# Kernel tuning notes

Hardware: AMD Instinct MI355X
Metric: run time of the kernel (lower is better)

The kernel has to match this reference:

```python
import jax, jax.numpy as jnp
import numpy as np

B, Q, K, H = 4, 256, 256, 512
NEG = -1e9


def setup_inputs() -> dict:
    key = jax.random.key(0)
    ks = jax.random.split(key, 7)
    scale = 1.0 / np.sqrt(H)
    return {
        "query": jax.random.normal(ks[0], (B, Q, H), jnp.float32),
        "key": jax.random.normal(ks[1], (B, K, H), jnp.float32),
        "value": jax.random.normal(ks[2], (B, K, H), jnp.float32),
        "valid_lens": jax.random.randint(ks[3], (B,), 0, K, jnp.int32),
        "Wq": jax.random.normal(ks[4], (H, H), jnp.float32) * scale,
        "Wk": jax.random.normal(ks[5], (H, H), jnp.float32) * scale,
        "wv": jax.random.normal(ks[6], (H,), jnp.float32) * scale,
    }


def reference(query, key, value, valid_lens, Wq, Wk, wv):
    # projections (nn.Linear without bias)
    q = query @ Wq              # [B,Q,H]
    k = key @ Wk                # [B,K,H]
    # broadcast add + tanh: [B,Q,K,H]
    features = jnp.tanh(q[:, :, None, :] + k[:, None, :, :])
    # score projection w_v: [B,Q,K]
    scores = jnp.einsum("bqkh,h->bqk", features, wv)
    # sequence mask: positions >= valid_len masked out
    mask = jnp.arange(K)[None, :] >= valid_lens[:, None]   # [B,K]
    scores = jnp.where(mask[:, None, :], NEG, scores)
    attn = jax.nn.softmax(scores, axis=-1)                 # [B,Q,K]
    context = jnp.einsum("bqk,bkh->bqh", attn, value)      # [B,Q,H]
    return context
```

## Files before the change

kernel.cpp:

```cpp
#include <hip/hip_runtime.h>
#include <hip/hip_bf16.h>

#define B_ 4
#define Q_ 256
#define K_ 256
#define H_ 512
#define NEG (-1e9f)
#define PRESCALE 2.885390081777927f

typedef _Float16 half8 __attribute__((ext_vector_type(8)));
typedef float    f32x4 __attribute__((ext_vector_type(4)));

__global__ __launch_bounds__(512) void proj_kernel(
    const float* __restrict__ Xq, const float* __restrict__ Xk,
    const float* __restrict__ Wq, const float* __restrict__ Wk,
    float* __restrict__ Eq, float* __restrict__ EkT,
    const int* __restrict__ vlen)
{
    const int bx   = blockIdx.x;
    const int z    = bx >> 4;
    const int row0 = (bx & 15) * 64;
    const int bb   = row0 >> 8;
    const int k0   = row0 & 255;
    if (z && k0 >= vlen[bb]) return;

    const float* X = z ? Xk : Xq;
    const float* W = z ? Wk : Wq;

    __shared__ _Float16 Xl[2][8 * 520];
    __shared__ _Float16 Wl[2][8 * 520];

    const int col0 = blockIdx.y * 64;
    const int t    = threadIdx.x;
    const int lane = t & 63;
    const int wave = t >> 6;
    const int mw   = wave >> 1;
    const int nw   = wave & 1;
    const int m    = lane & 15;
    const int kgl  = lane >> 4;

    const int xr = t >> 3;
    const int xg = t & 7;
    const int wc = t & 63;
    const int wg = t >> 6;

    f32x4 acc[2] = {};

    float4 xv0 = *(const float4*)&X[(size_t)(row0 + xr) * H_ + xg * 8];
    float4 xv1 = *(const float4*)&X[(size_t)(row0 + xr) * H_ + xg * 8 + 4];
    float wv8[8];
    #pragma unroll
    for (int i = 0; i < 8; ++i)
        wv8[i] = W[(size_t)(wg * 8 + i) * H_ + col0 + wc];

    for (int it = 0; it < 8; ++it) {
        const int buf = it & 1;
        {
            half8 hx;
            hx[0] = (_Float16)xv0.x; hx[1] = (_Float16)xv0.y;
            hx[2] = (_Float16)xv0.z; hx[3] = (_Float16)xv0.w;
            hx[4] = (_Float16)xv1.x; hx[5] = (_Float16)xv1.y;
            hx[6] = (_Float16)xv1.z; hx[7] = (_Float16)xv1.w;
            *(half8*)&Xl[buf][xg * 520 + xr * 8] = hx;
            half8 hw;
            #pragma unroll
            for (int i = 0; i < 8; ++i) hw[i] = (_Float16)wv8[i];
            *(half8*)&Wl[buf][wg * 520 + wc * 8] = hw;
        }
        __syncthreads();
        if (it < 7) {
            const int kk = (it + 1) * 64;
            xv0 = *(const float4*)&X[(size_t)(row0 + xr) * H_ + kk + xg * 8];
            xv1 = *(const float4*)&X[(size_t)(row0 + xr) * H_ + kk + xg * 8 + 4];
            #pragma unroll
            for (int i = 0; i < 8; ++i)
                wv8[i] = W[(size_t)(kk + wg * 8 + i) * H_ + col0 + wc];
        }
        const _Float16* Asrc = z ? &Wl[buf][0] : &Xl[buf][0];
        const _Float16* Bsrc = z ? &Xl[buf][0] : &Wl[buf][0];
        #pragma unroll
        for (int ks = 0; ks < 2; ++ks) {
            const int slab = (ks * 4 + kgl) * 520;
            const half8 af = *(const half8*)&Asrc[slab + (16 * mw + m) * 8];
            #pragma unroll
            for (int nt = 0; nt < 2; ++nt) {
                const half8 bf =
                    *(const half8*)&Bsrc[slab + (nw * 32 + nt * 16 + m) * 8];
                acc[nt] = __builtin_amdgcn_mfma_f32_16x16x32_f16(af, bf, acc[nt], 0, 0, 0);
            }
        }
    }

    const int rloc = 16 * mw + kgl * 4;
    if (!z) {
        #pragma unroll
        for (int nt = 0; nt < 2; ++nt) {
            const int gcol = col0 + nw * 32 + nt * 16 + m;
            #pragma unroll
            for (int r = 0; r < 4; ++r)
                Eq[(size_t)(row0 + rloc + r) * H_ + gcol] =
                    __builtin_amdgcn_exp2f(acc[nt][r] * PRESCALE);
        }
    } else {
        #pragma unroll
        for (int nt = 0; nt < 2; ++nt) {
            const int gk = k0 + nw * 32 + nt * 16 + m;
            #pragma unroll
            for (int r = 0; r < 4; ++r)
                EkT[((size_t)bb * H_ + col0 + rloc + r) * K_ + gk] =
                    __builtin_amdgcn_exp2f(acc[nt][r] * PRESCALE);
        }
    }
}

__global__ __launch_bounds__(512) void fused_attn(
    const float* __restrict__ Eq, const float* __restrict__ EkT,
    const float* __restrict__ value, const int* __restrict__ vlen,
    const float* __restrict__ wv, float* __restrict__ out)
{
    const int qt = blockIdx.x;
    const int b  = blockIdx.y;
    const int q0 = qt * 2;
    const int t    = threadIdx.x;
    const int wave = t >> 6;
    const int lane = t & 63;

    __shared__ float eqh2[8 * 132];
    __shared__ float wm2[8 * 68];
    __shared__ float sc[2][K_];
    __shared__ float ctxp[4][2][H_];

    const int valid = vlen[b];

    if (t < 256) {
        const int qi = t >> 7, p4 = (t & 127) * 4;
        const float4 v = *(const float4*)&Eq[((size_t)b * Q_ + q0 + qi) * H_ + p4];
        const float vv[4] = {v.x, v.y, v.z, v.w};
        #pragma unroll
        for (int j = 0; j < 4; ++j) {
            const int h = p4 + j;
            eqh2[(h & 7) * 132 + (h >> 3) * 2 + qi] = vv[j];
        }
    } else if (t < 384) {
        const int i = (t - 256) * 4;
        const float4 w = *(const float4*)&wv[i];
        const float ww[4] = {w.x, w.y, w.z, w.w};
        #pragma unroll
        for (int j = 0; j < 4; ++j) {
            const int h = i + j;
            wm2[(h & 7) * 68 + (h >> 3)] = -2.f * ww[j];
        }
    }
    __syncthreads();

    const int band = wave * 32;
    const int ho   = lane >> 3;
    const int kg   = lane & 7;
    const int kq   = band + kg * 4;

    if (band < valid) {
        const float* ekp = EkT + ((size_t)b * H_ + ho) * K_ + kq;
        float a0[4] = {}, a1[4] = {};
        float4 pe[4], n1[4], n2[4];
        #pragma unroll
        for (int p = 0; p < 4; ++p)
            pe[p] = *(const float4*)(ekp + (size_t)p * 8 * K_);
        #pragma unroll
        for (int p = 0; p < 4; ++p)
            n1[p] = *(const float4*)(ekp + (size_t)(4 + p) * 8 * K_);

        for (int g = 0; g < 16; ++g) {
            if (g < 14) {
                #pragma unroll
                for (int p = 0; p < 4; ++p)
                    n2[p] = *(const float4*)(ekp + (size_t)((g + 2) * 4 + p) * 8 * K_);
            }
            const float4 eqA = *(const float4*)&eqh2[ho * 132 + g * 8];
            const float4 eqB = *(const float4*)&eqh2[ho * 132 + g * 8 + 4];
            const float4 wv4 = *(const float4*)&wm2[ho * 68 + g * 4];
            const float eq0[4] = {eqA.x, eqA.z, eqB.x, eqB.z};
            const float eq1[4] = {eqA.y, eqA.w, eqB.y, eqB.w};
            const float wmp[4] = {wv4.x, wv4.y, wv4.z, wv4.w};
            #pragma unroll
            for (int p = 0; p < 4; ++p) {
                const float ek4[4] = {pe[p].x, pe[p].y, pe[p].z, pe[p].w};
                #pragma unroll
                for (int j = 0; j < 4; ++j) {
                    const float g0 = __builtin_fmaf(eq0[p], ek4[j], 1.0f);
                    a0[j] = __builtin_fmaf(wmp[p], __builtin_amdgcn_rcpf(g0), a0[j]);
                    const float g1 = __builtin_fmaf(eq1[p], ek4[j], 1.0f);
                    a1[j] = __builtin_fmaf(wmp[p], __builtin_amdgcn_rcpf(g1), a1[j]);
                }
            }
            #pragma unroll
            for (int p = 0; p < 4; ++p) { pe[p] = n1[p]; n1[p] = n2[p]; }
        }
        #pragma unroll
        for (int d = 8; d < 64; d <<= 1) {
            #pragma unroll
            for (int j = 0; j < 4; ++j) {
                a0[j] += __shfl_xor(a0[j], d);
                a1[j] += __shfl_xor(a1[j], d);
            }
        }
        if (ho == 0) {
            *(float4*)&sc[0][kq] = make_float4(a0[0], a0[1], a0[2], a0[3]);
            *(float4*)&sc[1][kq] = make_float4(a1[0], a1[1], a1[2], a1[3]);
        }
    }
    __syncthreads();

    if (wave < 2) {
        const int q = wave;
        if (valid == 0) {
            #pragma unroll
            for (int j = 0; j < 4; ++j) sc[q][lane + 64 * j] = 1.0f / K_;
        } else {
            float sv[4], mx = -3e38f;
            #pragma unroll
            for (int j = 0; j < 4; ++j) {
                const int kk = lane + 64 * j;
                const float s = (kk < valid) ? sc[q][kk] : NEG;
                sv[j] = s;
                mx = fmaxf(mx, s);
            }
            #pragma unroll
            for (int d = 32; d; d >>= 1) mx = fmaxf(mx, __shfl_xor(mx, d));
            float ev[4], sum = 0.f;
            #pragma unroll
            for (int j = 0; j < 4; ++j) { ev[j] = __expf(sv[j] - mx); sum += ev[j]; }
            #pragma unroll
            for (int d = 32; d; d >>= 1) sum += __shfl_xor(sum, d);
            const float inv = 1.0f / sum;
            #pragma unroll
            for (int j = 0; j < 4; ++j) sc[q][lane + 64 * j] = ev[j] * inv;
        }
    }
    __syncthreads();

    const int klim = (valid == 0) ? K_ : valid;
    const int kb   = wave * 32;
    const int kend = min(32, klim - kb);
    const int h0   = lane * 8;

    float c0[8] = {}, c1[8] = {};
    for (int kc = 0; kc < kend; ++kc) {
        const int kk = kb + kc;
        const float4* vp = (const float4*)&value[((size_t)b * K_ + kk) * H_ + h0];
        const float4 v0 = vp[0], v1 = vp[1];
        const float vr[8] = {v0.x, v0.y, v0.z, v0.w, v1.x, v1.y, v1.z, v1.w};
        const float a0 = sc[0][kk], a1 = sc[1][kk];
        #pragma unroll
        for (int j = 0; j < 8; ++j) {
            c0[j] = __builtin_fmaf(a0, vr[j], c0[j]);
            c1[j] = __builtin_fmaf(a1, vr[j], c1[j]);
        }
    }

    #define PARK(s)                                                         \
        do {                                                                \
            float* d0 = &ctxp[s][0][h0];                                    \
            float* d1 = &ctxp[s][1][h0];                                    \
            ((float4*)d0)[0] = make_float4(c0[0], c0[1], c0[2], c0[3]);     \
            ((float4*)d0)[1] = make_float4(c0[4], c0[5], c0[6], c0[7]);     \
            ((float4*)d1)[0] = make_float4(c1[0], c1[1], c1[2], c1[3]);     \
            ((float4*)d1)[1] = make_float4(c1[4], c1[5], c1[6], c1[7]);     \
        } while (0)
    #define FOLD(s)                                                         \
        do {                                                                \
            const float* d0 = &ctxp[s][0][h0];                              \
            const float* d1 = &ctxp[s][1][h0];                              \
            _Pragma("unroll")                                               \
            for (int j = 0; j < 8; ++j) { c0[j] += d0[j]; c1[j] += d1[j]; } \
        } while (0)

    if (wave >= 4) PARK(wave - 4);
    __syncthreads();
    if (wave < 4) FOLD(wave);
    __syncthreads();
    if (wave == 2 || wave == 3) PARK(wave - 2);
    __syncthreads();
    if (wave < 2) FOLD(wave);
    __syncthreads();
    if (wave == 1) PARK(1);
    __syncthreads();
    if (wave == 0) {
        FOLD(1);
        float* o0 = &out[((size_t)b * Q_ + q0 + 0) * H_ + h0];
        float* o1 = &out[((size_t)b * Q_ + q0 + 1) * H_ + h0];
        ((float4*)o0)[0] = make_float4(c0[0], c0[1], c0[2], c0[3]);
        ((float4*)o0)[1] = make_float4(c0[4], c0[5], c0[6], c0[7]);
        ((float4*)o1)[0] = make_float4(c1[0], c1[1], c1[2], c1[3]);
        ((float4*)o1)[1] = make_float4(c1[4], c1[5], c1[6], c1[7]);
    }
    #undef PARK
    #undef FOLD
}

extern "C" void kernel_launch(void* const* d_in, const int* in_sizes, int n_in,
                              void* d_out, int out_size, void* d_ws, size_t ws_size,
                              hipStream_t stream)
{
    const float* query = (const float*)d_in[0];
    const float* key   = (const float*)d_in[1];
    const float* value = (const float*)d_in[2];
    const int*   vlen  = (const int*)  d_in[3];
    const float* Wq    = (const float*)d_in[4];
    const float* Wk    = (const float*)d_in[5];
    const float* wv    = (const float*)d_in[6];
    float*       outp  = (float*)d_out;

    float* EqBuf  = (float*)d_ws;
    float* EkTBuf = EqBuf + (size_t)B_ * Q_ * H_;

    dim3 g1(32, 8);
    proj_kernel<<<g1, 512, 0, stream>>>(query, key, Wq, Wk, EqBuf, EkTBuf, vlen);

    dim3 g2(Q_ / 2, B_);
    fused_attn<<<g2, 512, 0, stream>>>(EqBuf, EkTBuf, value, vlen, wv, outp);
}
```

Measured before the change: 37.11 us.

## Process four queries per block in fused attention to reuse Ek loads

Each fused_attn block now handles four query rows instead of two, halving the grid. Every EkT element loaded from global memory is reused for four queries in the tanh-score loop, and value rows are reused for four context rows in the PV stage. The Eq shared-memory layout is interleaved by four to allow a single float4 LDS read per h. In exchange, each thread holds twice the accumulator registers, which may reduce occupancy, and the smaller grid (256 blocks) gives less parallelism across CUs.

```diff
diff --git a/kernel.cpp b/kernel.cpp
--- a/kernel.cpp
+++ b/kernel.cpp
@@ -120,35 +120,34 @@
 {
     const int qt = blockIdx.x;
     const int b  = blockIdx.y;
-    const int q0 = qt * 2;
+    const int q0 = qt * 4;
     const int t    = threadIdx.x;
     const int wave = t >> 6;
     const int lane = t & 63;
 
-    __shared__ float eqh2[8 * 132];
+    __shared__ float eqh2[8 * 260];
     __shared__ float wm2[8 * 68];
-    __shared__ float sc[2][K_];
-    __shared__ float ctxp[4][2][H_];
+    __shared__ float sc[4][K_];
+    __shared__ float ctxp[4][4][H_];
 
     const int valid = vlen[b];
 
-    if (t < 256) {
+    {
         const int qi = t >> 7, p4 = (t & 127) * 4;
         const float4 v = *(const float4*)&Eq[((size_t)b * Q_ + q0 + qi) * H_ + p4];
         const float vv[4] = {v.x, v.y, v.z, v.w};
-        #pragma unroll
-        for (int j = 0; j < 4; ++j) {
-            const int h = p4 + j;
-            eqh2[(h & 7) * 132 + (h >> 3) * 2 + qi] = vv[j];
-        }
-    } else if (t < 384) {
-        const int i = (t - 256) * 4;
-        const float4 w = *(const float4*)&wv[i];
-        const float ww[4] = {w.x, w.y, w.z, w.w};
-        #pragma unroll
-        for (int j = 0; j < 4; ++j) {
-            const int h = i + j;
-            wm2[(h & 7) * 68 + (h >> 3)] = -2.f * ww[j];
+        const int sbase = (p4 >> 3) * 4;
+        #pragma unroll
+        for (int j = 0; j < 4; ++j)
+            eqh2[((p4 & 7) + j) * 260 + sbase + qi] = vv[j];
+        if (t < 128) {
+            const float4 w = *(const float4*)&wv[t * 4];
+            const float ww[4] = {w.x, w.y, w.z, w.w};
+            #pragma unroll
+            for (int j = 0; j < 4; ++j) {
+                const int h = t * 4 + j;
+                wm2[(h & 7) * 68 + (h >> 3)] = -2.f * ww[j];
+            }
         }
     }
     __syncthreads();
@@ -160,7 +159,7 @@
 
     if (band < valid) {
         const float* ekp = EkT + ((size_t)b * H_ + ho) * K_ + kq;
-        float a0[4] = {}, a1[4] = {};
+        float acc0[4] = {}, acc1[4] = {}, acc2[4] = {}, acc3[4] = {};
         float4 pe[4], n1[4], n2[4];
         #pragma unroll
         for (int p = 0; p < 4; ++p)
@@ -175,21 +174,22 @@
                 for (int p = 0; p < 4; ++p)
                     n2[p] = *(const float4*)(ekp + (size_t)((g + 2) * 4 + p) * 8 * K_);
             }
-            const float4 eqA = *(const float4*)&eqh2[ho * 132 + g * 8];
-            const float4 eqB = *(const float4*)&eqh2[ho * 132 + g * 8 + 4];
             const float4 wv4 = *(const float4*)&wm2[ho * 68 + g * 4];
-            const float eq0[4] = {eqA.x, eqA.z, eqB.x, eqB.z};
-            const float eq1[4] = {eqA.y, eqA.w, eqB.y, eqB.w};
             const float wmp[4] = {wv4.x, wv4.y, wv4.z, wv4.w};
             #pragma unroll
             for (int p = 0; p < 4; ++p) {
+                const float4 eq4 = *(const float4*)&eqh2[ho * 260 + (g * 4 + p) * 4];
                 const float ek4[4] = {pe[p].x, pe[p].y, pe[p].z, pe[p].w};
                 #pragma unroll
                 for (int j = 0; j < 4; ++j) {
-                    const float g0 = __builtin_fmaf(eq0[p], ek4[j], 1.0f);
-                    a0[j] = __builtin_fmaf(wmp[p], __builtin_amdgcn_rcpf(g0), a0[j]);
-                    const float g1 = __builtin_fmaf(eq1[p], ek4[j], 1.0f);
-                    a1[j] = __builtin_fmaf(wmp[p], __builtin_amdgcn_rcpf(g1), a1[j]);
+                    const float g0 = __builtin_fmaf(eq4.x, ek4[j], 1.0f);
+                    acc0[j] = __builtin_fmaf(wmp[p], __builtin_amdgcn_rcpf(g0), acc0[j]);
+                    const float g1 = __builtin_fmaf(eq4.y, ek4[j], 1.0f);
+                    acc1[j] = __builtin_fmaf(wmp[p], __builtin_amdgcn_rcpf(g1), acc1[j]);
+                    const float g2 = __builtin_fmaf(eq4.z, ek4[j], 1.0f);
+                    acc2[j] = __builtin_fmaf(wmp[p], __builtin_amdgcn_rcpf(g2), acc2[j]);
+                    const float g3 = __builtin_fmaf(eq4.w, ek4[j], 1.0f);
+                    acc3[j] = __builtin_fmaf(wmp[p], __builtin_amdgcn_rcpf(g3), acc3[j]);
                 }
             }
             #pragma unroll
@@ -199,18 +199,22 @@
         for (int d = 8; d < 64; d <<= 1) {
             #pragma unroll
             for (int j = 0; j < 4; ++j) {
-                a0[j] += __shfl_xor(a0[j], d);
-                a1[j] += __shfl_xor(a1[j], d);
+                acc0[j] += __shfl_xor(acc0[j], d);
+                acc1[j] += __shfl_xor(acc1[j], d);
+                acc2[j] += __shfl_xor(acc2[j], d);
+                acc3[j] += __shfl_xor(acc3[j], d);
             }
         }
         if (ho == 0) {
-            *(float4*)&sc[0][kq] = make_float4(a0[0], a0[1], a0[2], a0[3]);
-            *(float4*)&sc[1][kq] = make_float4(a1[0], a1[1], a1[2], a1[3]);
-        }
-    }
-    __syncthreads();
-
-    if (wave < 2) {
+            *(float4*)&sc[0][kq] = make_float4(acc0[0], acc0[1], acc0[2], acc0[3]);
+            *(float4*)&sc[1][kq] = make_float4(acc1[0], acc1[1], acc1[2], acc1[3]);
+            *(float4*)&sc[2][kq] = make_float4(acc2[0], acc2[1], acc2[2], acc2[3]);
+            *(float4*)&sc[3][kq] = make_float4(acc3[0], acc3[1], acc3[2], acc3[3]);
+        }
+    }
+    __syncthreads();
+
+    if (wave < 4) {
         const int q = wave;
         if (valid == 0) {
             #pragma unroll
@@ -243,35 +247,39 @@
     const int kend = min(32, klim - kb);
     const int h0   = lane * 8;
 
-    float c0[8] = {}, c1[8] = {};
+    float c[4][8] = {};
     for (int kc = 0; kc < kend; ++kc) {
         const int kk = kb + kc;
         const float4* vp = (const float4*)&value[((size_t)b * K_ + kk) * H_ + h0];
         const float4 v0 = vp[0], v1 = vp[1];
         const float vr[8] = {v0.x, v0.y, v0.z, v0.w, v1.x, v1.y, v1.z, v1.w};
-        const float a0 = sc[0][kk], a1 = sc[1][kk];
+        const float a0 = sc[0][kk], a1 = sc[1][kk], a2 = sc[2][kk], a3 = sc[3][kk];
         #pragma unroll
         for (int j = 0; j < 8; ++j) {
-            c0[j] = __builtin_fmaf(a0, vr[j], c0[j]);
-            c1[j] = __builtin_fmaf(a1, vr[j], c1[j]);
-        }
-    }
-
-    #define PARK(s)                                                         \
-        do {                                                                \
-            float* d0 = &ctxp[s][0][h0];                                    \
-            float* d1 = &ctxp[s][1][h0];                                    \
-            ((float4*)d0)[0] = make_float4(c0[0], c0[1], c0[2], c0[3]);     \
-            ((float4*)d0)[1] = make_float4(c0[4], c0[5], c0[6], c0[7]);     \
-            ((float4*)d1)[0] = make_float4(c1[0], c1[1], c1[2], c1[3]);     \
-            ((float4*)d1)[1] = make_float4(c1[4], c1[5], c1[6], c1[7]);     \
+            c[0][j] = __builtin_fmaf(a0, vr[j], c[0][j]);
+            c[1][j] = __builtin_fmaf(a1, vr[j], c[1][j]);
+            c[2][j] = __builtin_fmaf(a2, vr[j], c[2][j]);
+            c[3][j] = __builtin_fmaf(a3, vr[j], c[3][j]);
+        }
+    }
+
+    #define PARK(s)                                                           \
+        do {                                                                  \
+            _Pragma("unroll")                                                 \
+            for (int qi = 0; qi < 4; ++qi) {                                  \
+                float* d = &ctxp[s][qi][h0];                                  \
+                ((float4*)d)[0] = make_float4(c[qi][0], c[qi][1], c[qi][2], c[qi][3]); \
+                ((float4*)d)[1] = make_float4(c[qi][4], c[qi][5], c[qi][6], c[qi][7]); \
+            }                                                                 \
         } while (0)
-    #define FOLD(s)                                                         \
-        do {                                                                \
-            const float* d0 = &ctxp[s][0][h0];                              \
-            const float* d1 = &ctxp[s][1][h0];                              \
-            _Pragma("unroll")                                               \
-            for (int j = 0; j < 8; ++j) { c0[j] += d0[j]; c1[j] += d1[j]; } \
+    #define FOLD(s)                                                           \
+        do {                                                                  \
+            _Pragma("unroll")                                                 \
+            for (int qi = 0; qi < 4; ++qi) {                                  \
+                const float* d = &ctxp[s][qi][h0];                            \
+                _Pragma("unroll")                                             \
+                for (int j = 0; j < 8; ++j) c[qi][j] += d[j];                 \
+            }                                                                 \
         } while (0)
 
     if (wave >= 4) PARK(wave - 4);
@@ -286,12 +294,12 @@
     __syncthreads();
     if (wave == 0) {
         FOLD(1);
-        float* o0 = &out[((size_t)b * Q_ + q0 + 0) * H_ + h0];
-        float* o1 = &out[((size_t)b * Q_ + q0 + 1) * H_ + h0];
-        ((float4*)o0)[0] = make_float4(c0[0], c0[1], c0[2], c0[3]);
-        ((float4*)o0)[1] = make_float4(c0[4], c0[5], c0[6], c0[7]);
-        ((float4*)o1)[0] = make_float4(c1[0], c1[1], c1[2], c1[3]);
-        ((float4*)o1)[1] = make_float4(c1[4], c1[5], c1[6], c1[7]);
+        #pragma unroll
+        for (int qi = 0; qi < 4; ++qi) {
+            float* o = &out[((size_t)b * Q_ + q0 + qi) * H_ + h0];
+            ((float4*)o)[0] = make_float4(c[qi][0], c[qi][1], c[qi][2], c[qi][3]);
+            ((float4*)o)[1] = make_float4(c[qi][4], c[qi][5], c[qi][6], c[qi][7]);
+        }
     }
     #undef PARK
     #undef FOLD
@@ -316,6 +324,6 @@
     dim3 g1(32, 8);
     proj_kernel<<<g1, 512, 0, stream>>>(query, key, Wq, Wk, EqBuf, EkTBuf, vlen);
 
-    dim3 g2(Q_ / 2, B_);
+    dim3 g2(Q_ / 4, B_);
     fused_attn<<<g2, 512, 0, stream>>>(EqBuf, EkTBuf, value, vlen, wv, outp);
 }
```

Result: no change. 36.65 us (-1.2%).
